# Performance work log

Hardware: AMD Instinct MI355X
Metric: run time of the kernel (lower is better)

## Reference

```python
import jax, jax.numpy as jnp
import numpy as np

N = 100000
E = 1600000
D_IN = 64
D_HID = 64
D_OUT = 64


def setup_inputs() -> dict:
    key = jax.random.key(0)
    ks = jax.random.split(key, 12)
    x = jax.random.normal(ks[0], (N, D_IN), dtype=jnp.float32)
    edge_index = jax.random.randint(ks[1], (2, E), 0, N, dtype=jnp.int64)
    s1 = 1.0 / np.sqrt(D_IN)
    s2 = 1.0 / np.sqrt(D_HID)
    return {
        "x": x,
        "edge_index": edge_index,
        "W1l": jax.random.uniform(ks[2], (D_HID, D_IN), jnp.float32, -s1, s1),
        "b1l": jax.random.uniform(ks[3], (D_HID,), jnp.float32, -s1, s1),
        "W1r": jax.random.uniform(ks[4], (D_HID, D_IN), jnp.float32, -s1, s1),
        "W2l": jax.random.uniform(ks[5], (D_HID, D_HID), jnp.float32, -s2, s2),
        "b2l": jax.random.uniform(ks[6], (D_HID,), jnp.float32, -s2, s2),
        "W2r": jax.random.uniform(ks[7], (D_HID, D_HID), jnp.float32, -s2, s2),
        "Wout": jax.random.uniform(ks[8], (D_OUT, D_HID), jnp.float32, -s2, s2),
        "bout": jax.random.uniform(ks[9], (D_OUT,), jnp.float32, -s2, s2),
        "drop": 0,
    }


def _sage_conv(x, src, dst, Wl, bl, Wr, n_nodes):
    # PyG SAGEConv, aggr='mean': out = lin_l(mean_j x_j) + lin_r(x_i)
    msg = x[src]                                            # [E, d] gather
    agg = jax.ops.segment_sum(msg, dst, num_segments=n_nodes)
    deg = jax.ops.segment_sum(jnp.ones((src.shape[0],), x.dtype), dst,
                              num_segments=n_nodes)
    mean = agg / jnp.maximum(deg, 1.0)[:, None]             # empty neighborhoods -> 0
    return mean @ Wl.T + bl + x @ Wr.T


def reference(x, edge_index, W1l, b1l, W1r, W2l, b2l, W2r, Wout, bout, drop):
    src, dst = edge_index[0], edge_index[1]
    n = x.shape[0]
    # dropout is identity in eval mode (training=False); drop unused
    h = jax.nn.relu(_sage_conv(x, src, dst, W1l, b1l, W1r, n))
    h = jax.nn.relu(_sage_conv(h, src, dst, W2l, b2l, W2r, n))
    logits = h @ Wout.T + bout
    return jax.nn.log_softmax(logits, axis=1)
```

## Files before the change

kernel.cpp:

```cpp
#include <hip/hip_runtime.h>


#define TB 256
#define TBA 1024
#define CAPB 2560

typedef __attribute__((ext_vector_type(8))) short bf16x8;
typedef __attribute__((ext_vector_type(4))) float f32x4;
typedef __attribute__((ext_vector_type(2))) float f32x2;

__device__ __forceinline__ unsigned short bf16c(float f) {
  union { float f; unsigned u; } v; v.f = f;
  unsigned r = (v.u + 0x7FFFu + ((v.u >> 16) & 1u)) >> 16;
  return (unsigned short)r;
}

__device__ __forceinline__ bf16x8 ld_bf8(const float* p) {
  float4 a = *(const float4*)p;
  float4 b = *(const float4*)(p + 4);
  bf16x8 r;
  r[0] = bf16c(a.x); r[1] = bf16c(a.y); r[2] = bf16c(a.z); r[3] = bf16c(a.w);
  r[4] = bf16c(b.x); r[5] = bf16c(b.y); r[6] = bf16c(b.z); r[7] = bf16c(b.w);
  return r;
}

__device__ __forceinline__ float bflo(unsigned u) { return __uint_as_float(u << 16); }
__device__ __forceinline__ float bfhi(unsigned u) { return __uint_as_float(u & 0xFFFF0000u); }
__device__ __forceinline__ unsigned bfpk(float lo, float hi) {
  return (unsigned)bf16c(lo) | ((unsigned)bf16c(hi) << 16);
}

__global__ __launch_bounds__(1024) void k_binA(
    const int* __restrict__ ei, int E,
    int* __restrict__ bucket_fill, unsigned int* __restrict__ bucketData, int NB) {
  __shared__ int hist[1024];
  __shared__ int base[1024];
  __shared__ int s_nz;
  if (threadIdx.x == 0) s_nz = 0;
  for (int i = threadIdx.x; i < NB; i += TBA) hist[i] = 0;
  __syncthreads();
  int nz = 0;
  for (int i = threadIdx.x; i < 2048; i += TBA) nz |= ei[2 * i + 1];
  if (nz) atomicOr(&s_nz, 1);
  __syncthreads();
  bool m64 = (s_nz == 0);

  long long e0 = (long long)E * blockIdx.x / gridDim.x;
  long long e1 = (long long)E * (blockIdx.x + 1) / gridDim.x;
  for (long long e = e0 + threadIdx.x; e < e1; e += TBA) {
    int dst = m64 ? ((const int2*)ei)[(long long)E + e].x : ei[(long long)E + e];
    atomicAdd(&hist[dst >> 7], 1);
  }
  __syncthreads();
  for (int b = threadIdx.x; b < NB; b += TBA) {
    int c = hist[b];
    base[b] = c ? atomicAdd(&bucket_fill[b], c) : 0;
    hist[b] = 0;
  }
  __syncthreads();
  for (long long e = e0 + threadIdx.x; e < e1; e += TBA) {
    int src, dst;
    if (m64) {
      src = ((const int2*)ei)[e].x;
      dst = ((const int2*)ei)[(long long)E + e].x;
    } else {
      src = ei[e];
      dst = ei[(long long)E + e];
    }
    int b = dst >> 7;
    int pos = base[b] + atomicAdd(&hist[b], 1);
    if (pos < CAPB)
      bucketData[(size_t)b * CAPB + pos] =
          ((unsigned)(dst & 127) << 24) | (unsigned)src;
  }
}

__global__ __launch_bounds__(256) void k_binB(
    const unsigned int* __restrict__ bucketData, const int* __restrict__ bucket_fill,
    int* __restrict__ colp, int* __restrict__ cnt) {
  __shared__ unsigned int slice[128 * 64];
  __shared__ int lcnt[128];
  int b = blockIdx.x;
  for (int i = threadIdx.x; i < 128; i += TB) lcnt[i] = 0;
  __syncthreads();
  int fcnt = bucket_fill[b];
  if (fcnt > CAPB) fcnt = CAPB;
  const unsigned int* bd = bucketData + (size_t)b * CAPB;
  for (int k = threadIdx.x; k < fcnt; k += TB) {
    unsigned int rec = bd[k];
    int dl = rec >> 24;
    int pos = atomicAdd(&lcnt[dl], 1);
    if (pos < 64) slice[(dl << 6) + pos] = rec & 0xFFFFFFu;
  }
  __syncthreads();
  size_t obase = (size_t)b * (128 * 64);
  for (int i = threadIdx.x * 4; i < 128 * 64; i += TB * 4) {
    *(uint4*)(colp + obase + i) = *(const uint4*)(slice + i);
  }
  int node0 = b << 7;
  for (int i = threadIdx.x; i < 128; i += TB) cnt[node0 + i] = lcnt[i];
}

__global__ __launch_bounds__(256) void k_xform_f32(
    const float* __restrict__ xin, const float* __restrict__ Wl,
    const float* __restrict__ Wr, const float* __restrict__ bl,
    unsigned short* __restrict__ y, unsigned short* __restrict__ zout, int n) {
  int lane = threadIdx.x & 63;
  int quad = lane >> 4, m = lane & 15;
  int w0 = (blockIdx.x * blockDim.x + threadIdx.x) >> 6;
  int nw = (gridDim.x * blockDim.x) >> 6;

  bf16x8 bfrag[8][2];
  float bias[4];
#pragma unroll
  for (int t = 0; t < 8; ++t) {
    const float* W = (t < 4) ? Wl : Wr;
    int row = (t & 3) * 16 + m;
#pragma unroll
    for (int s = 0; s < 2; ++s)
      bfrag[t][s] = ld_bf8(W + row * 64 + s * 32 + quad * 8);
  }
#pragma unroll
  for (int t = 0; t < 4; ++t) bias[t] = bl[t * 16 + m];

  int nT = (n + 15) >> 4;
  for (int tile = w0; tile < nT; tile += nw) {
    int node0 = tile << 4;
    int mrow = node0 + m;
    if (mrow >= n) mrow = n - 1;
    const float* xr = xin + (size_t)mrow * 64;
    bf16x8 a0 = ld_bf8(xr + quad * 8);
    bf16x8 a1 = ld_bf8(xr + 32 + quad * 8);

    f32x4 acc[8];
#pragma unroll
    for (int t = 0; t < 8; ++t) {
      f32x4 z4 = {0.f, 0.f, 0.f, 0.f};
      z4 = __builtin_amdgcn_mfma_f32_16x16x32_bf16(a0, bfrag[t][0], z4, 0, 0, 0);
      acc[t] = __builtin_amdgcn_mfma_f32_16x16x32_bf16(a1, bfrag[t][1], z4, 0, 0, 0);
    }

#pragma unroll
    for (int r = 0; r < 4; ++r) {
      int node = node0 + quad * 4 + r;
      if (node >= n) break;
      size_t rb = (size_t)node * 64 + m;
#pragma unroll
      for (int t = 0; t < 4; ++t) y[rb + t * 16] = bf16c(acc[t][r]);
#pragma unroll
      for (int t = 0; t < 4; ++t) zout[rb + t * 16] = bf16c(acc[t + 4][r] + bias[t]);
    }
  }
}

__global__ __launch_bounds__(256) void k_xform_b16(
    const unsigned short* zin, const float* __restrict__ Wl,
    const float* __restrict__ Wr, const float* __restrict__ bl,
    unsigned short* __restrict__ y, unsigned short* zout, int n) {
  int lane = threadIdx.x & 63;
  int quad = lane >> 4, m = lane & 15;
  int w0 = (blockIdx.x * blockDim.x + threadIdx.x) >> 6;
  int nw = (gridDim.x * blockDim.x) >> 6;

  bf16x8 bfrag[8][2];
  float bias[4];
#pragma unroll
  for (int t = 0; t < 8; ++t) {
    const float* W = (t < 4) ? Wl : Wr;
    int row = (t & 3) * 16 + m;
#pragma unroll
    for (int s = 0; s < 2; ++s)
      bfrag[t][s] = ld_bf8(W + row * 64 + s * 32 + quad * 8);
  }
#pragma unroll
  for (int t = 0; t < 4; ++t) bias[t] = bl[t * 16 + m];

  int nT = (n + 15) >> 4;
  for (int tile = w0; tile < nT; tile += nw) {
    int node0 = tile << 4;
    int mrow = node0 + m;
    if (mrow >= n) mrow = n - 1;
    const unsigned short* xr = zin + (size_t)mrow * 64;
    bf16x8 a0 = *(const bf16x8*)(xr + quad * 8);
    bf16x8 a1 = *(const bf16x8*)(xr + 32 + quad * 8);

    f32x4 acc[8];
#pragma unroll
    for (int t = 0; t < 8; ++t) {
      f32x4 z4 = {0.f, 0.f, 0.f, 0.f};
      z4 = __builtin_amdgcn_mfma_f32_16x16x32_bf16(a0, bfrag[t][0], z4, 0, 0, 0);
      acc[t] = __builtin_amdgcn_mfma_f32_16x16x32_bf16(a1, bfrag[t][1], z4, 0, 0, 0);
    }

#pragma unroll
    for (int r = 0; r < 4; ++r) {
      int node = node0 + quad * 4 + r;
      if (node >= n) break;
      size_t rb = (size_t)node * 64 + m;
#pragma unroll
      for (int t = 0; t < 4; ++t) y[rb + t * 16] = bf16c(acc[t][r]);
#pragma unroll
      for (int t = 0; t < 4; ++t) zout[rb + t * 16] = bf16c(acc[t + 4][r] + bias[t]);
    }
  }
}

__global__ __launch_bounds__(256) void k_aggr(
    const unsigned short* __restrict__ yb, const int* __restrict__ cnt,
    const int* __restrict__ colp, unsigned short* zio, int n) {
  const unsigned int* y = (const unsigned int*)yb;
  int lane = threadIdx.x & 63;
  int wv = (blockIdx.x * blockDim.x + threadIdx.x) >> 6;
  int g16 = lane & 48;
  int lig = lane & 15;
  int sub = lig >> 3;
  int fo = (lig & 7) * 4;

  int node = (wv << 2) + (g16 >> 4);
  bool act = node < n;
  int cn = act ? node : 0;
  int deg = cnt[cn];
  int jcap = deg < 64 ? deg : 64;
  size_t crow = (size_t)cn << 6;
  int cidxA = colp[crow + lig];
  int cidxB = colp[crow + 16 + lig];

  int wmax = jcap;
  wmax = max(wmax, __shfl_xor(wmax, 16, 64));
  wmax = max(wmax, __shfl_xor(wmax, 32, 64));

  f32x2 acc[4];
#pragma unroll
  for (int k = 0; k < 4; ++k) acc[k] = (f32x2){0.f, 0.f};

#define ACCUM(U)                                             \
  do {                                                       \
    acc[0] += (f32x2){bflo((U).x), bfhi((U).x)};             \
    acc[1] += (f32x2){bflo((U).y), bfhi((U).y)};             \
    acc[2] += (f32x2){bflo((U).z), bfhi((U).z)};             \
    acc[3] += (f32x2){bflo((U).w), bfhi((U).w)};             \
  } while (0)

  {
    int lim = wmax < 16 ? wmax : 16;
    for (int s = 0; s < lim; s += 2) {
      int slot = s + sub;
      int c = __shfl(cidxA, g16 | slot, 64);
      if (slot < jcap) {
        uint4 v = *(const uint4*)(y + ((size_t)c << 5) + fo);
        ACCUM(v);
      }
    }
  }
  if (wmax > 16) {
    int lim = (wmax < 32 ? wmax : 32) - 16;
    for (int s = 0; s < lim; s += 2) {
      int slot = s + sub;
      int c = __shfl(cidxB, g16 | slot, 64);
      if (slot + 16 < jcap) {
        uint4 v = *(const uint4*)(y + ((size_t)c << 5) + fo);
        ACCUM(v);
      }
    }
  }
  if (wmax > 32) {
    int cidxC = colp[crow + 32 + lig];
    int cidxD = colp[crow + 48 + lig];
    {
      int lim = (wmax < 48 ? wmax : 48) - 32;
      for (int s = 0; s < lim; s += 2) {
        int slot = s + sub;
        int c = __shfl(cidxC, g16 | slot, 64);
        if (slot + 32 < jcap) {
          uint4 v = *(const uint4*)(y + ((size_t)c << 5) + fo);
          ACCUM(v);
        }
      }
    }
    if (wmax > 48) {
      int lim = wmax - 48;
      for (int s = 0; s < lim; s += 2) {
        int slot = s + sub;
        int c = __shfl(cidxD, g16 | slot, 64);
        if (slot + 48 < jcap) {
          uint4 v = *(const uint4*)(y + ((size_t)c << 5) + fo);
          ACCUM(v);
        }
      }
    }
  }
#undef ACCUM

#pragma unroll
  for (int k = 0; k < 4; ++k) {
    acc[k].x += __shfl_xor(acc[k].x, 8, 64);
    acc[k].y += __shfl_xor(acc[k].y, 8, 64);
  }

  if (act && sub == 0) {
    float inv = (deg > 0) ? 1.0f / (float)deg : 0.f;
    unsigned int* zp = (unsigned int*)(zio + ((size_t)node << 6)) + fo;
    uint4 zv = *(uint4*)zp;
    zv.x = bfpk(fmaxf(fmaf(acc[0].x, inv, bflo(zv.x)), 0.f),
                fmaxf(fmaf(acc[0].y, inv, bfhi(zv.x)), 0.f));
    zv.y = bfpk(fmaxf(fmaf(acc[1].x, inv, bflo(zv.y)), 0.f),
                fmaxf(fmaf(acc[1].y, inv, bfhi(zv.y)), 0.f));
    zv.z = bfpk(fmaxf(fmaf(acc[2].x, inv, bflo(zv.z)), 0.f),
                fmaxf(fmaf(acc[2].y, inv, bfhi(zv.z)), 0.f));
    zv.w = bfpk(fmaxf(fmaf(acc[3].x, inv, bflo(zv.w)), 0.f),
                fmaxf(fmaf(acc[3].y, inv, bfhi(zv.w)), 0.f));
    *(uint4*)zp = zv;
  }
}

__global__ __launch_bounds__(256) void k_out(
    const unsigned short* __restrict__ h, const float* __restrict__ Wo,
    const float* __restrict__ bo, float* __restrict__ out, int n) {
  int lane = threadIdx.x & 63;
  int quad = lane >> 4, m = lane & 15;
  int w0 = (blockIdx.x * blockDim.x + threadIdx.x) >> 6;
  int nw = (gridDim.x * blockDim.x) >> 6;

  bf16x8 bfrag[4][2];
  float bias[4];
#pragma unroll
  for (int t = 0; t < 4; ++t) {
    int row = t * 16 + m;
#pragma unroll
    for (int s = 0; s < 2; ++s)
      bfrag[t][s] = ld_bf8(Wo + row * 64 + s * 32 + quad * 8);
    bias[t] = bo[t * 16 + m];
  }

  int nT = (n + 15) >> 4;
  for (int tile = w0; tile < nT; tile += nw) {
    int node0 = tile << 4;
    int mrow = node0 + m;
    if (mrow >= n) mrow = n - 1;
    const unsigned short* xr = h + (size_t)mrow * 64;
    bf16x8 a0 = *(const bf16x8*)(xr + quad * 8);
    bf16x8 a1 = *(const bf16x8*)(xr + 32 + quad * 8);

    f32x4 acc[4];
#pragma unroll
    for (int t = 0; t < 4; ++t) {
      f32x4 z4 = {0.f, 0.f, 0.f, 0.f};
      z4 = __builtin_amdgcn_mfma_f32_16x16x32_bf16(a0, bfrag[t][0], z4, 0, 0, 0);
      acc[t] = __builtin_amdgcn_mfma_f32_16x16x32_bf16(a1, bfrag[t][1], z4, 0, 0, 0);
    }

#pragma unroll
    for (int r = 0; r < 4; ++r) {
      int node = node0 + quad * 4 + r;
      if (node >= n) break;
      float l0 = acc[0][r] + bias[0];
      float l1 = acc[1][r] + bias[1];
      float l2 = acc[2][r] + bias[2];
      float l3 = acc[3][r] + bias[3];
      float mx = fmaxf(fmaxf(l0, l1), fmaxf(l2, l3));
#pragma unroll
      for (int off = 1; off <= 8; off <<= 1) mx = fmaxf(mx, __shfl_xor(mx, off, 64));
      float s = expf(l0 - mx) + expf(l1 - mx) + expf(l2 - mx) + expf(l3 - mx);
#pragma unroll
      for (int off = 1; off <= 8; off <<= 1) s += __shfl_xor(s, off, 64);
      float ls = logf(s);
      size_t rb = (size_t)node * 64 + m;
      out[rb + 0]  = l0 - mx - ls;
      out[rb + 16] = l1 - mx - ls;
      out[rb + 32] = l2 - mx - ls;
      out[rb + 48] = l3 - mx - ls;
    }
  }
}

extern "C" void kernel_launch(void* const* d_in, const int* in_sizes, int n_in,
                              void* d_out, int out_size, void* d_ws, size_t ws_size,
                              hipStream_t stream) {
  const float* x    = (const float*)d_in[0];
  const int*   ei   = (const int*)d_in[1];
  const float* W1l  = (const float*)d_in[2];
  const float* b1l  = (const float*)d_in[3];
  const float* W1r  = (const float*)d_in[4];
  const float* W2l  = (const float*)d_in[5];
  const float* b2l  = (const float*)d_in[6];
  const float* W2r  = (const float*)d_in[7];
  const float* Wout = (const float*)d_in[8];
  const float* bout = (const float*)d_in[9];
  int N = in_sizes[0] / 64;
  int E = in_sizes[1] / 2;
  int NB = (N + 127) >> 7;

  char* p = (char*)d_ws;
  auto carve = [&](size_t bytes) {
    char* r = p;
    p += (bytes + 255) & ~(size_t)255;
    return r;
  };
  int* bucket_fill   = (int*)carve((size_t)NB * 4);
  int* cnt           = (int*)carve((size_t)NB * 128 * 4);
  int* colp          = (int*)carve((size_t)NB * 128 * 64 * 4);
  unsigned short* y  = (unsigned short*)carve((size_t)N * 64 * 2);
  unsigned short* z  = (unsigned short*)carve((size_t)N * 64 * 2);
  unsigned int* bucketData = (unsigned int*)z;

  hipMemsetAsync(bucket_fill, 0, (size_t)NB * 4, stream);

  k_binA<<<256, TBA, 0, stream>>>(ei, E, bucket_fill, bucketData, NB);
  k_binB<<<NB, TB, 0, stream>>>(bucketData, bucket_fill, colp, cnt);

  int aggr_blocks = (N + 15) / 16;
  k_xform_f32<<<512, TB, 0, stream>>>(x, W1l, W1r, b1l, y, z, N);
  k_aggr<<<aggr_blocks, TB, 0, stream>>>(y, cnt, colp, z, N);
  k_xform_b16<<<512, TB, 0, stream>>>(z, W2l, W2r, b2l, y, z, N);
  k_aggr<<<aggr_blocks, TB, 0, stream>>>(y, cnt, colp, z, N);
  k_out<<<512, TB, 0, stream>>>(z, Wout, bout, (float*)d_out, N);
}
```

Measured before the change: 241.4 us.

## Replace two-pass bucket binning with direct atomic CSR fill fused into layer-1 transform

```diff
diff --git a/kernel.cpp b/kernel.cpp
--- a/kernel.cpp
+++ b/kernel.cpp
@@ -2,8 +2,8 @@
 
 
 #define TB 256
-#define TBA 1024
-#define CAPB 2560
+#define NBIN 256
+#define XFB 512
 
 typedef __attribute__((ext_vector_type(8))) short bf16x8;
 typedef __attribute__((ext_vector_type(4))) float f32x4;
@@ -30,85 +30,53 @@
   return (unsigned)bf16c(lo) | ((unsigned)bf16c(hi) << 16);
 }
 
-__global__ __launch_bounds__(1024) void k_binA(
+__global__ __launch_bounds__(256) void k_bin_xf(
     const int* __restrict__ ei, int E,
-    int* __restrict__ bucket_fill, unsigned int* __restrict__ bucketData, int NB) {
-  __shared__ int hist[1024];
-  __shared__ int base[1024];
-  __shared__ int s_nz;
-  if (threadIdx.x == 0) s_nz = 0;
-  for (int i = threadIdx.x; i < NB; i += TBA) hist[i] = 0;
-  __syncthreads();
-  int nz = 0;
-  for (int i = threadIdx.x; i < 2048; i += TBA) nz |= ei[2 * i + 1];
-  if (nz) atomicOr(&s_nz, 1);
-  __syncthreads();
-  bool m64 = (s_nz == 0);
-
-  long long e0 = (long long)E * blockIdx.x / gridDim.x;
-  long long e1 = (long long)E * (blockIdx.x + 1) / gridDim.x;
-  for (long long e = e0 + threadIdx.x; e < e1; e += TBA) {
-    int dst = m64 ? ((const int2*)ei)[(long long)E + e].x : ei[(long long)E + e];
-    atomicAdd(&hist[dst >> 7], 1);
-  }
-  __syncthreads();
-  for (int b = threadIdx.x; b < NB; b += TBA) {
-    int c = hist[b];
-    base[b] = c ? atomicAdd(&bucket_fill[b], c) : 0;
-    hist[b] = 0;
-  }
-  __syncthreads();
-  for (long long e = e0 + threadIdx.x; e < e1; e += TBA) {
-    int src, dst;
-    if (m64) {
-      src = ((const int2*)ei)[e].x;
-      dst = ((const int2*)ei)[(long long)E + e].x;
-    } else {
-      src = ei[e];
-      dst = ei[(long long)E + e];
-    }
-    int b = dst >> 7;
-    int pos = base[b] + atomicAdd(&hist[b], 1);
-    if (pos < CAPB)
-      bucketData[(size_t)b * CAPB + pos] =
-          ((unsigned)(dst & 127) << 24) | (unsigned)src;
-  }
-}
-
-__global__ __launch_bounds__(256) void k_binB(
-    const unsigned int* __restrict__ bucketData, const int* __restrict__ bucket_fill,
-    int* __restrict__ colp, int* __restrict__ cnt) {
-  __shared__ unsigned int slice[128 * 64];
-  __shared__ int lcnt[128];
-  int b = blockIdx.x;
-  for (int i = threadIdx.x; i < 128; i += TB) lcnt[i] = 0;
-  __syncthreads();
-  int fcnt = bucket_fill[b];
-  if (fcnt > CAPB) fcnt = CAPB;
-  const unsigned int* bd = bucketData + (size_t)b * CAPB;
-  for (int k = threadIdx.x; k < fcnt; k += TB) {
-    unsigned int rec = bd[k];
-    int dl = rec >> 24;
-    int pos = atomicAdd(&lcnt[dl], 1);
-    if (pos < 64) slice[(dl << 6) + pos] = rec & 0xFFFFFFu;
-  }
-  __syncthreads();
-  size_t obase = (size_t)b * (128 * 64);
-  for (int i = threadIdx.x * 4; i < 128 * 64; i += TB * 4) {
-    *(uint4*)(colp + obase + i) = *(const uint4*)(slice + i);
-  }
-  int node0 = b << 7;
-  for (int i = threadIdx.x; i < 128; i += TB) cnt[node0 + i] = lcnt[i];
-}
-
-__global__ __launch_bounds__(256) void k_xform_f32(
+    int* __restrict__ cnt, int* __restrict__ colp,
     const float* __restrict__ xin, const float* __restrict__ Wl,
     const float* __restrict__ Wr, const float* __restrict__ bl,
     unsigned short* __restrict__ y, unsigned short* __restrict__ zout, int n) {
+  if (blockIdx.x < NBIN) {
+    __shared__ int s_nz;
+    if (threadIdx.x == 0) s_nz = 0;
+    __syncthreads();
+    int nz = 0;
+    for (int i = threadIdx.x; i < 2048; i += TB) nz |= ei[2 * i + 1];
+    if (nz) atomicOr(&s_nz, 1);
+    __syncthreads();
+    bool m64 = (s_nz == 0);
+    int bb = blockIdx.x;
+    if (m64) {
+      long long e0 = ((long long)E * bb / NBIN) & ~1LL;
+      long long e1 = ((long long)E * (bb + 1) / NBIN) & ~1LL;
+      if (bb == NBIN - 1) e1 = E;
+      for (long long e = e0 + (long long)threadIdx.x * 2; e < e1; e += TB * 2) {
+        int4 sp = *(const int4*)(ei + (e << 1));
+        int4 dp = *(const int4*)(ei + (((long long)E + e) << 1));
+        int pos0 = atomicAdd(&cnt[dp.x], 1);
+        if (pos0 < 64) colp[((size_t)dp.x << 6) + pos0] = sp.x;
+        if (e + 1 < e1) {
+          int pos1 = atomicAdd(&cnt[dp.z], 1);
+          if (pos1 < 64) colp[((size_t)dp.z << 6) + pos1] = sp.z;
+        }
+      }
+    } else {
+      long long e0 = (long long)E * bb / NBIN;
+      long long e1 = (long long)E * (bb + 1) / NBIN;
+      for (long long e = e0 + threadIdx.x; e < e1; e += TB) {
+        int src = ei[e];
+        int dst = ei[(long long)E + e];
+        int pos = atomicAdd(&cnt[dst], 1);
+        if (pos < 64) colp[((size_t)dst << 6) + pos] = src;
+      }
+    }
+    return;
+  }
+
   int lane = threadIdx.x & 63;
   int quad = lane >> 4, m = lane & 15;
-  int w0 = (blockIdx.x * blockDim.x + threadIdx.x) >> 6;
-  int nw = (gridDim.x * blockDim.x) >> 6;
+  int w0 = ((blockIdx.x - NBIN) * TB + threadIdx.x) >> 6;
+  int nw = (XFB * TB) >> 6;
 
   bf16x8 bfrag[8][2];
   float bias[4];
@@ -241,20 +209,18 @@
     acc[3] += (f32x2){bflo((U).w), bfhi((U).w)};             \
   } while (0)
 
-  {
-    int lim = wmax < 16 ? wmax : 16;
-    for (int s = 0; s < lim; s += 2) {
-      int slot = s + sub;
-      int c = __shfl(cidxA, g16 | slot, 64);
-      if (slot < jcap) {
-        uint4 v = *(const uint4*)(y + ((size_t)c << 5) + fo);
-        ACCUM(v);
-      }
+#pragma unroll
+  for (int s = 0; s < 16; s += 2) {
+    int slot = s + sub;
+    int c = __shfl(cidxA, g16 | slot, 64);
+    if (slot < jcap) {
+      uint4 v = *(const uint4*)(y + ((size_t)c << 5) + fo);
+      ACCUM(v);
     }
   }
   if (wmax > 16) {
-    int lim = (wmax < 32 ? wmax : 32) - 16;
-    for (int s = 0; s < lim; s += 2) {
+#pragma unroll
+    for (int s = 0; s < 16; s += 2) {
       int slot = s + sub;
       int c = __shfl(cidxB, g16 | slot, 64);
       if (slot + 16 < jcap) {
@@ -396,22 +362,17 @@
     p += (bytes + 255) & ~(size_t)255;
     return r;
   };
-  int* bucket_fill   = (int*)carve((size_t)NB * 4);
   int* cnt           = (int*)carve((size_t)NB * 128 * 4);
   int* colp          = (int*)carve((size_t)NB * 128 * 64 * 4);
   unsigned short* y  = (unsigned short*)carve((size_t)N * 64 * 2);
   unsigned short* z  = (unsigned short*)carve((size_t)N * 64 * 2);
-  unsigned int* bucketData = (unsigned int*)z;
-
-  hipMemsetAsync(bucket_fill, 0, (size_t)NB * 4, stream);
-
-  k_binA<<<256, TBA, 0, stream>>>(ei, E, bucket_fill, bucketData, NB);
-  k_binB<<<NB, TB, 0, stream>>>(bucketData, bucket_fill, colp, cnt);
+
+  hipMemsetAsync(cnt, 0, (size_t)N * 4, stream);
 
   int aggr_blocks = (N + 15) / 16;
-  k_xform_f32<<<512, TB, 0, stream>>>(x, W1l, W1r, b1l, y, z, N);
+  k_bin_xf<<<NBIN + XFB, TB, 0, stream>>>(ei, E, cnt, colp, x, W1l, W1r, b1l, y, z, N);
   k_aggr<<<aggr_blocks, TB, 0, stream>>>(y, cnt, colp, z, N);
-  k_xform_b16<<<512, TB, 0, stream>>>(z, W2l, W2r, b2l, y, z, N);
+  k_xform_b16<<<XFB, TB, 0, stream>>>(z, W2l, W2r, b2l, y, z, N);
   k_aggr<<<aggr_blocks, TB, 0, stream>>>(y, cnt, colp, z, N);
-  k_out<<<512, TB, 0, stream>>>(z, Wout, bout, (float*)d_out, N);
-}
+  k_out<<<XFB, TB, 0, stream>>>(z, Wout, bout, (float*)d_out, N);
+}
```

New measurement: 272.7 us. 13.0% more time.

## Fuse edge binning with first-layer transform into one heterogeneous kernel launch

Applied to the files above, without the earlier changes.

```diff
diff --git a/kernel.cpp b/kernel.cpp
--- a/kernel.cpp
+++ b/kernel.cpp
@@ -2,7 +2,8 @@
 
 
 #define TB 256
-#define TBA 1024
+#define NBINA 256
+#define XFB 512
 #define CAPB 2560
 
 typedef __attribute__((ext_vector_type(8))) short bf16x8;
@@ -30,48 +31,102 @@
   return (unsigned)bf16c(lo) | ((unsigned)bf16c(hi) << 16);
 }
 
-__global__ __launch_bounds__(1024) void k_binA(
+__global__ __launch_bounds__(256) void k_binA_xf(
     const int* __restrict__ ei, int E,
-    int* __restrict__ bucket_fill, unsigned int* __restrict__ bucketData, int NB) {
-  __shared__ int hist[1024];
-  __shared__ int base[1024];
-  __shared__ int s_nz;
-  if (threadIdx.x == 0) s_nz = 0;
-  for (int i = threadIdx.x; i < NB; i += TBA) hist[i] = 0;
-  __syncthreads();
-  int nz = 0;
-  for (int i = threadIdx.x; i < 2048; i += TBA) nz |= ei[2 * i + 1];
-  if (nz) atomicOr(&s_nz, 1);
-  __syncthreads();
-  bool m64 = (s_nz == 0);
-
-  long long e0 = (long long)E * blockIdx.x / gridDim.x;
-  long long e1 = (long long)E * (blockIdx.x + 1) / gridDim.x;
-  for (long long e = e0 + threadIdx.x; e < e1; e += TBA) {
-    int dst = m64 ? ((const int2*)ei)[(long long)E + e].x : ei[(long long)E + e];
-    atomicAdd(&hist[dst >> 7], 1);
-  }
-  __syncthreads();
-  for (int b = threadIdx.x; b < NB; b += TBA) {
-    int c = hist[b];
-    base[b] = c ? atomicAdd(&bucket_fill[b], c) : 0;
-    hist[b] = 0;
-  }
-  __syncthreads();
-  for (long long e = e0 + threadIdx.x; e < e1; e += TBA) {
-    int src, dst;
-    if (m64) {
-      src = ((const int2*)ei)[e].x;
-      dst = ((const int2*)ei)[(long long)E + e].x;
-    } else {
-      src = ei[e];
-      dst = ei[(long long)E + e];
-    }
-    int b = dst >> 7;
-    int pos = base[b] + atomicAdd(&hist[b], 1);
-    if (pos < CAPB)
-      bucketData[(size_t)b * CAPB + pos] =
-          ((unsigned)(dst & 127) << 24) | (unsigned)src;
+    int* __restrict__ bucket_fill, unsigned int* __restrict__ bucketData, int NB,
+    const float* __restrict__ xin, const float* __restrict__ Wl,
+    const float* __restrict__ Wr, const float* __restrict__ bl,
+    unsigned short* __restrict__ y, unsigned short* __restrict__ zout, int n) {
+  if (blockIdx.x < NBINA) {
+    __shared__ int hist[1024];
+    __shared__ int base[1024];
+    __shared__ int s_nz;
+    if (threadIdx.x == 0) s_nz = 0;
+    for (int i = threadIdx.x; i < NB; i += TB) hist[i] = 0;
+    __syncthreads();
+    int nz = 0;
+    for (int i = threadIdx.x; i < 2048; i += TB) nz |= ei[2 * i + 1];
+    if (nz) atomicOr(&s_nz, 1);
+    __syncthreads();
+    bool m64 = (s_nz == 0);
+    int bb = blockIdx.x;
+
+    long long e0 = (long long)E * bb / NBINA;
+    long long e1 = (long long)E * (bb + 1) / NBINA;
+    for (long long e = e0 + threadIdx.x; e < e1; e += TB) {
+      int dst = m64 ? ((const int2*)ei)[(long long)E + e].x : ei[(long long)E + e];
+      atomicAdd(&hist[dst >> 7], 1);
+    }
+    __syncthreads();
+    for (int b = threadIdx.x; b < NB; b += TB) {
+      int c = hist[b];
+      base[b] = c ? atomicAdd(&bucket_fill[b], c) : 0;
+      hist[b] = 0;
+    }
+    __syncthreads();
+    for (long long e = e0 + threadIdx.x; e < e1; e += TB) {
+      int src, dst;
+      if (m64) {
+        src = ((const int2*)ei)[e].x;
+        dst = ((const int2*)ei)[(long long)E + e].x;
+      } else {
+        src = ei[e];
+        dst = ei[(long long)E + e];
+      }
+      int b = dst >> 7;
+      int pos = base[b] + atomicAdd(&hist[b], 1);
+      if (pos < CAPB)
+        bucketData[(size_t)b * CAPB + pos] =
+            ((unsigned)(dst & 127) << 24) | (unsigned)src;
+    }
+    return;
+  }
+
+  int lane = threadIdx.x & 63;
+  int quad = lane >> 4, m = lane & 15;
+  int w0 = ((blockIdx.x - NBINA) * TB + threadIdx.x) >> 6;
+  int nw = (XFB * TB) >> 6;
+
+  bf16x8 bfrag[8][2];
+  float bias[4];
+#pragma unroll
+  for (int t = 0; t < 8; ++t) {
+    const float* W = (t < 4) ? Wl : Wr;
+    int row = (t & 3) * 16 + m;
+#pragma unroll
+    for (int s = 0; s < 2; ++s)
+      bfrag[t][s] = ld_bf8(W + row * 64 + s * 32 + quad * 8);
+  }
+#pragma unroll
+  for (int t = 0; t < 4; ++t) bias[t] = bl[t * 16 + m];
+
+  int nT = (n + 15) >> 4;
+  for (int tile = w0; tile < nT; tile += nw) {
+    int node0 = tile << 4;
+    int mrow = node0 + m;
+    if (mrow >= n) mrow = n - 1;
+    const float* xr = xin + (size_t)mrow * 64;
+    bf16x8 a0 = ld_bf8(xr + quad * 8);
+    bf16x8 a1 = ld_bf8(xr + 32 + quad * 8);
+
+    f32x4 acc[8];
+#pragma unroll
+    for (int t = 0; t < 8; ++t) {
+      f32x4 z4 = {0.f, 0.f, 0.f, 0.f};
+      z4 = __builtin_amdgcn_mfma_f32_16x16x32_bf16(a0, bfrag[t][0], z4, 0, 0, 0);
+      acc[t] = __builtin_amdgcn_mfma_f32_16x16x32_bf16(a1, bfrag[t][1], z4, 0, 0, 0);
+    }
+
+#pragma unroll
+    for (int r = 0; r < 4; ++r) {
+      int node = node0 + quad * 4 + r;
+      if (node >= n) break;
+      size_t rb = (size_t)node * 64 + m;
+#pragma unroll
+      for (int t = 0; t < 4; ++t) y[rb + t * 16] = bf16c(acc[t][r]);
+#pragma unroll
+      for (int t = 0; t < 4; ++t) zout[rb + t * 16] = bf16c(acc[t + 4][r] + bias[t]);
+    }
   }
 }
 
@@ -101,58 +156,6 @@
   for (int i = threadIdx.x; i < 128; i += TB) cnt[node0 + i] = lcnt[i];
 }
 
-__global__ __launch_bounds__(256) void k_xform_f32(
-    const float* __restrict__ xin, const float* __restrict__ Wl,
-    const float* __restrict__ Wr, const float* __restrict__ bl,
-    unsigned short* __restrict__ y, unsigned short* __restrict__ zout, int n) {
-  int lane = threadIdx.x & 63;
-  int quad = lane >> 4, m = lane & 15;
-  int w0 = (blockIdx.x * blockDim.x + threadIdx.x) >> 6;
-  int nw = (gridDim.x * blockDim.x) >> 6;
-
-  bf16x8 bfrag[8][2];
-  float bias[4];
-#pragma unroll
-  for (int t = 0; t < 8; ++t) {
-    const float* W = (t < 4) ? Wl : Wr;
-    int row = (t & 3) * 16 + m;
-#pragma unroll
-    for (int s = 0; s < 2; ++s)
-      bfrag[t][s] = ld_bf8(W + row * 64 + s * 32 + quad * 8);
-  }
-#pragma unroll
-  for (int t = 0; t < 4; ++t) bias[t] = bl[t * 16 + m];
-
-  int nT = (n + 15) >> 4;
-  for (int tile = w0; tile < nT; tile += nw) {
-    int node0 = tile << 4;
-    int mrow = node0 + m;
-    if (mrow >= n) mrow = n - 1;
-    const float* xr = xin + (size_t)mrow * 64;
-    bf16x8 a0 = ld_bf8(xr + quad * 8);
-    bf16x8 a1 = ld_bf8(xr + 32 + quad * 8);
-
-    f32x4 acc[8];
-#pragma unroll
-    for (int t = 0; t < 8; ++t) {
-      f32x4 z4 = {0.f, 0.f, 0.f, 0.f};
-      z4 = __builtin_amdgcn_mfma_f32_16x16x32_bf16(a0, bfrag[t][0], z4, 0, 0, 0);
-      acc[t] = __builtin_amdgcn_mfma_f32_16x16x32_bf16(a1, bfrag[t][1], z4, 0, 0, 0);
-    }
-
-#pragma unroll
-    for (int r = 0; r < 4; ++r) {
-      int node = node0 + quad * 4 + r;
-      if (node >= n) break;
-      size_t rb = (size_t)node * 64 + m;
-#pragma unroll
-      for (int t = 0; t < 4; ++t) y[rb + t * 16] = bf16c(acc[t][r]);
-#pragma unroll
-      for (int t = 0; t < 4; ++t) zout[rb + t * 16] = bf16c(acc[t + 4][r] + bias[t]);
-    }
-  }
-}
-
 __global__ __launch_bounds__(256) void k_xform_b16(
     const unsigned short* zin, const float* __restrict__ Wl,
     const float* __restrict__ Wr, const float* __restrict__ bl,
@@ -241,20 +244,18 @@
     acc[3] += (f32x2){bflo((U).w), bfhi((U).w)};             \
   } while (0)
 
-  {
-    int lim = wmax < 16 ? wmax : 16;
-    for (int s = 0; s < lim; s += 2) {
-      int slot = s + sub;
-      int c = __shfl(cidxA, g16 | slot, 64);
-      if (slot < jcap) {
-        uint4 v = *(const uint4*)(y + ((size_t)c << 5) + fo);
-        ACCUM(v);
-      }
+#pragma unroll
+  for (int s = 0; s < 16; s += 2) {
+    int slot = s + sub;
+    int c = __shfl(cidxA, g16 | slot, 64);
+    if (slot < jcap) {
+      uint4 v = *(const uint4*)(y + ((size_t)c << 5) + fo);
+      ACCUM(v);
     }
   }
   if (wmax > 16) {
-    int lim = (wmax < 32 ? wmax : 32) - 16;
-    for (int s = 0; s < lim; s += 2) {
+#pragma unroll
+    for (int s = 0; s < 16; s += 2) {
       int slot = s + sub;
       int c = __shfl(cidxB, g16 | slot, 64);
       if (slot + 16 < jcap) {
@@ -401,17 +402,16 @@
   int* colp          = (int*)carve((size_t)NB * 128 * 64 * 4);
   unsigned short* y  = (unsigned short*)carve((size_t)N * 64 * 2);
   unsigned short* z  = (unsigned short*)carve((size_t)N * 64 * 2);
-  unsigned int* bucketData = (unsigned int*)z;
+  unsigned int* bucketData = (unsigned int*)carve((size_t)NB * CAPB * 4);
 
   hipMemsetAsync(bucket_fill, 0, (size_t)NB * 4, stream);
 
-  k_binA<<<256, TBA, 0, stream>>>(ei, E, bucket_fill, bucketData, NB);
+  int aggr_blocks = (N + 15) / 16;
+  k_binA_xf<<<NBINA + XFB, TB, 0, stream>>>(ei, E, bucket_fill, bucketData, NB,
+                                            x, W1l, W1r, b1l, y, z, N);
   k_binB<<<NB, TB, 0, stream>>>(bucketData, bucket_fill, colp, cnt);
-
-  int aggr_blocks = (N + 15) / 16;
-  k_xform_f32<<<512, TB, 0, stream>>>(x, W1l, W1r, b1l, y, z, N);
   k_aggr<<<aggr_blocks, TB, 0, stream>>>(y, cnt, colp, z, N);
-  k_xform_b16<<<512, TB, 0, stream>>>(z, W2l, W2r, b2l, y, z, N);
+  k_xform_b16<<<XFB, TB, 0, stream>>>(z, W2l, W2r, b2l, y, z, N);
   k_aggr<<<aggr_blocks, TB, 0, stream>>>(y, cnt, colp, z, N);
-  k_out<<<512, TB, 0, stream>>>(z, Wout, bout, (float*)d_out, N);
-}
+  k_out<<<XFB, TB, 0, stream>>>(z, Wout, bout, (float*)d_out, N);
+}
```

Measured after the change: 243.4 us. Within noise of the previous version (+0.9%).
